# Kernel tuning notes

Hardware: AMD Instinct MI355X
Metric: run time of the kernel (lower is better)

## Reference

```python
import jax, jax.numpy as jnp
import numpy as np

RADIUS = 2.0  # ball-query radius (float forward arg in the original; fixed here)


def _conv1x1(x, W, b):
    # 1x1 Conv2D over NHWC == per-point linear layer
    return jnp.einsum('bmsc,cd->bmsd', x, W) + b


def _ball_query(xyz, new_xyz, radius, nsample):
    """For each cluster center, take the first (by index) nsample points within
    radius, padding with the first found neighbor (TF ball-query semantics).
    xyz: (B,N,3), new_xyz: (B,M,3) -> idx (B,M,nsample) int32."""
    N = xyz.shape[1]
    d2 = jnp.sum((new_xyz[:, :, None, :] - xyz[:, None, :, :]) ** 2, axis=-1)  # (B,M,N)
    valid = d2 < radius * radius
    key = jnp.where(valid, jnp.arange(N, dtype=jnp.int32)[None, None, :], N)
    order = jnp.argsort(key, axis=-1)[..., :nsample]          # (B,M,nsample)
    skey = jnp.take_along_axis(key, order, axis=-1)
    idx = jnp.where(skey < N, order, order[..., :1])          # pad with first neighbor
    return idx


def setup_inputs() -> dict:
    key = jax.random.key(0)
    ks = jax.random.split(key, 8)
    B, N = 8, 8192
    xyz = jax.random.normal(ks[0], (B, N, 3), dtype=jnp.float32)

    def w(k, cin, cout):
        return (jax.random.normal(k, (cin, cout), dtype=jnp.float32) / np.sqrt(cin)).astype(jnp.float32)

    z = lambda c: jnp.zeros((c,), jnp.float32)
    inp = {
        'xyz': xyz,
        'W1': w(ks[1], 3, 64),    'b1': z(64),
        'W2': w(ks[2], 64, 128),  'b2': z(128),
        'W3': w(ks[3], 128, 256), 'b3': z(256),
        'W4': w(ks[4], 256, 128), 'b4': z(128),
        'W5': w(ks[5], 128, 64),  'b5': z(64),
        'Wa': w(ks[6], 64, 1),    'ba': z(1),
        'Wo': w(ks[7], 64, 2),    'bo': z(2),
        'num_clusters': 512,
        'num_samples': 64,
    }
    return inp


def reference(xyz, W1, b1, W2, b2, W3, b3, W4, b4, W5, b5, Wa, ba, Wo, bo,
              num_clusters, num_samples):
    # sample cluster centers (deterministic stand-in for random subsampling)
    new_xyz = xyz[:, :num_clusters]                                    # (B,M,3)
    idx = _ball_query(xyz, new_xyz, RADIUS, num_samples)               # (B,M,S)
    grouped = jax.vmap(lambda pts, i: pts[i])(xyz, idx)                # (B,M,S,3)
    g = (grouped - new_xyz[:, :, None, :]) / RADIUS                    # normalize_radius

    # shared per-point MLP (1x1 convs, relu)
    h = jax.nn.relu(_conv1x1(g, W1, b1))
    h = jax.nn.relu(_conv1x1(h, W2, b2))
    h = jax.nn.relu(_conv1x1(h, W3, b3))
    # MaxPoolAxis: max over samples, keepdims
    h = jnp.max(h, axis=2, keepdims=True)                              # (B,M,1,256)
    # mlp2 convs (linear, no activation in source)
    h = _conv1x1(h, W4, b4)
    h = _conv1x1(h, W5, b5)                                            # (B,M,1,64)

    attention = jax.nn.softplus(_conv1x1(h, Wa, ba))[:, :, 0, 0]       # (B,M)
    o = _conv1x1(h, Wo, bo)[:, :, 0, :]                                # (B,M,2)
    o = o / jnp.sqrt(jnp.maximum(jnp.sum(o * o, axis=-1, keepdims=True), 1e-8))
    orientation = jnp.arctan2(o[..., 1], o[..., 0])                    # (B,M)
    return new_xyz, idx, attention, orientation
```

## Files before the change

kernel.cpp:

```cpp
#include <hip/hip_runtime.h>
#include <math.h>

#define BB 8
#define NN 8192
#define MM 512
#define SS 64
#define NCLUST (BB*MM)

#define OUT_IDX   (BB*MM*3)
#define OUT_ATT   (OUT_IDX + BB*MM*SS)
#define OUT_ORI   (OUT_ATT + BB*MM)

#define WS_W3 8192

typedef short v8s __attribute__((ext_vector_type(8)));
typedef float v4f __attribute__((ext_vector_type(4)));

static __device__ __forceinline__ unsigned short f2bf(float x) {
    unsigned int u = __float_as_uint(x);
    u += 0x7FFFu + ((u >> 16) & 1u);
    return (unsigned short)(u >> 16);
}

__global__ void pack_weights(const float* __restrict__ W2,
                             const float* __restrict__ W3,
                             unsigned short* __restrict__ ws)
{
    const int gid = blockIdx.x * 256 + threadIdx.x;
    const float* W; unsigned short* dst; int N, kt, nt, lane;
    if (gid < 1024) {
        W = W2; N = 128;
        const int tile = gid >> 6; lane = gid & 63;
        kt = tile >> 3; nt = tile & 7;
        dst = ws + (size_t)(tile * 64 + lane) * 8;
    } else {
        const int g = gid - 1024;
        W = W3; N = 256;
        const int tile = g >> 6; lane = g & 63;
        kt = tile >> 4; nt = tile & 15;
        dst = ws + WS_W3 + (size_t)(tile * 64 + lane) * 8;
    }
    const int k0 = kt * 32 + (lane >> 4) * 8;
    const int n  = nt * 16 + (lane & 15);
    union { unsigned short u[8]; v8s v; } f;
    #pragma unroll
    for (int j = 0; j < 8; ++j) f.u[j] = f2bf(W[(k0 + j) * N + n]);
    *(v8s*)dst = f.v;
}

__global__ __launch_bounds__(256, 4) void feat3d_fused(
    const float* __restrict__ xyz,
    const float* __restrict__ W1, const float* __restrict__ b1,
    const float* __restrict__ b2, const float* __restrict__ b3,
    const unsigned short* __restrict__ Wp,
    const float* __restrict__ W4, const float* __restrict__ b4,
    const float* __restrict__ W5, const float* __restrict__ b5,
    const float* __restrict__ Wa, const float* __restrict__ ba,
    const float* __restrict__ Wo, const float* __restrict__ bo,
    float* __restrict__ out)
{
    __shared__ __align__(16) unsigned char lds[24576];
    unsigned short* a2p = (unsigned short*)lds;
    unsigned short* a3p = (unsigned short*)(lds + 8192);
    float* smallf       = (float*)(lds + 8192);
    int* ls_idx         = (int*)(lds + 10240);
    unsigned long long* ls_mask = (unsigned long long*)(lds + 10496);

    float* ls_g  = smallf;
    float* ls_w1 = smallf + 256;

    float* vbuf   = (float*)lds;
    float* h4part = (float*)(lds + 1024);
    float* h4f    = (float*)(lds + 5120);
    float* h5p    = (float*)(lds + 5632);

    const int t   = threadIdx.x;
    const int wv  = t >> 6;
    const int l   = t & 63;
    const int q   = l >> 4;
    const int r16 = l & 15;
    const int blk = blockIdx.x;
    const int b   = blk >> 9;
    const int m   = blk & 511;
    const float* xb = xyz + (size_t)b * (NN * 3);

    const v8s* W2f = (const v8s*)Wp;
    v8s bfr[2][2];
    #pragma unroll
    for (int kt = 0; kt < 2; ++kt)
        #pragma unroll
        for (int ni = 0; ni < 2; ++ni)
            bfr[kt][ni] = W2f[(kt*8 + 2*wv + ni)*64 + l];

    const float cx = xb[m*3+0], cy = xb[m*3+1], cz = xb[m*3+2];

    if (t < 3) out[(b*MM + m)*3 + t] = xb[m*3 + t];

    if (t < 64) {
        ls_w1[t*4+0] = W1[t];
        ls_w1[t*4+1] = W1[64 + t];
        ls_w1[t*4+2] = W1[128 + t];
        ls_w1[t*4+3] = b1[t];
    }

    int cnt = 0;
    {
        int base = 0, pb = 0;
        while (base < NN && cnt < SS) {
            const int j = base + t;
            const float dx = xb[j*3+0] - cx;
            const float dy = xb[j*3+1] - cy;
            const float dz = xb[j*3+2] - cz;
            const float d2 = __fadd_rn(__fadd_rn(__fmul_rn(dx,dx), __fmul_rn(dy,dy)),
                                       __fmul_rn(dz,dz));
            const bool valid = d2 < 4.0f;
            const unsigned long long mask = __ballot(valid);
            if (l == 0) ls_mask[pb*4 + wv] = mask;
            __syncthreads();
            const unsigned long long m0 = ls_mask[pb*4+0], m1 = ls_mask[pb*4+1],
                                     m2 = ls_mask[pb*4+2], m3 = ls_mask[pb*4+3];
            int below = __popcll(mask & ((1ull << l) - 1ull));
            if (wv > 0) below += (int)__popcll(m0);
            if (wv > 1) below += (int)__popcll(m1);
            if (wv > 2) below += (int)__popcll(m2);
            const int pos = cnt + below;
            if (valid && pos < SS) {
                ls_idx[pos]   = j;
                ls_g[pos*4+0] = dx * 0.5f;
                ls_g[pos*4+1] = dy * 0.5f;
                ls_g[pos*4+2] = dz * 0.5f;
            }
            cnt += (int)(__popcll(m0) + __popcll(m1) + __popcll(m2) + __popcll(m3));
            if (cnt > SS) cnt = SS;
            base += 256;
            pb ^= 1;
        }
    }
    __syncthreads();
    if (t < SS && t >= cnt) {
        ls_idx[t]   = ls_idx[0];
        ls_g[t*4+0] = ls_g[0];
        ls_g[t*4+1] = ls_g[1];
        ls_g[t*4+2] = ls_g[2];
    }
    __syncthreads();
    if (t < 64) out[OUT_IDX + (b*MM + m)*SS + t] = (float)ls_idx[t];

    {
        const int s = wv*16 + r16;
        const float4 g4 = *(const float4*)&ls_g[s*4];
        #pragma unroll
        for (int kt = 0; kt < 2; ++kt) {
            union { unsigned short u[8]; v8s v; } fr;
            #pragma unroll
            for (int j = 0; j < 8; ++j) {
                const int c = kt*32 + q*8 + j;
                const float4 w = *(const float4*)&ls_w1[c*4];
                const float h = fmaf(g4.x, w.x, fmaf(g4.y, w.y, fmaf(g4.z, w.z, w.w)));
                fr.u[j] = f2bf(fmaxf(h, 0.f));
            }
            *(v8s*)&a2p[((kt*4 + wv)*64 + l)*8] = fr.v;
        }
    }
    __syncthreads();

    {
        const v4f z = {0.f, 0.f, 0.f, 0.f};
        v4f acc[4][2];
        #pragma unroll
        for (int mt = 0; mt < 4; ++mt) { acc[mt][0] = z; acc[mt][1] = z; }

        #pragma unroll
        for (int kt = 0; kt < 2; ++kt)
            #pragma unroll
            for (int mt = 0; mt < 4; ++mt) {
                const v8s a = *(const v8s*)&a2p[((kt*4 + mt)*64 + l)*8];
                #pragma unroll
                for (int ni = 0; ni < 2; ++ni)
                    acc[mt][ni] = __builtin_amdgcn_mfma_f32_16x16x32_bf16(
                        a, bfr[kt][ni], acc[mt][ni], 0, 0, 0);
            }

        #pragma unroll
        for (int ni = 0; ni < 2; ++ni) {
            const int c2  = (2*wv + ni)*16 + r16;
            const float bias = b2[c2];
            const int kt3 = c2 >> 5;
            const int lhi = ((c2 >> 3) & 3) << 4;
            const int j3  = c2 & 7;
            #pragma unroll
            for (int mt = 0; mt < 4; ++mt)
                #pragma unroll
                for (int rg = 0; rg < 4; ++rg) {
                    const float h = fmaxf(acc[mt][ni][rg] + bias, 0.f);
                    const int s15 = q*4 + rg;
                    a3p[((kt3*4 + mt)*64 + (lhi | s15))*8 + j3] = f2bf(h);
                }
        }
    }
    __syncthreads();

    {
        const v8s* W3f = (const v8s*)(Wp + WS_W3);

        #pragma unroll
        for (int np = 0; np < 2; ++np) {
            const int nt0 = 4*wv + 2*np;
            const v4f z = {0.f, 0.f, 0.f, 0.f};
            v4f acc[4][2];
            #pragma unroll
            for (int mt = 0; mt < 4; ++mt) { acc[mt][0] = z; acc[mt][1] = z; }

            v8s bb0 = W3f[(0*16 + nt0    )*64 + l];
            v8s bb1 = W3f[(0*16 + nt0 + 1)*64 + l];
            #pragma unroll
            for (int kt = 0; kt < 4; ++kt) {
                v8s a[4];
                #pragma unroll
                for (int mt = 0; mt < 4; ++mt)
                    a[mt] = *(const v8s*)&a3p[((kt*4 + mt)*64 + l)*8];
                v8s nb0, nb1;
                if (kt < 3) {
                    nb0 = W3f[((kt+1)*16 + nt0    )*64 + l];
                    nb1 = W3f[((kt+1)*16 + nt0 + 1)*64 + l];
                }
                #pragma unroll
                for (int mt = 0; mt < 4; ++mt) {
                    acc[mt][0] = __builtin_amdgcn_mfma_f32_16x16x32_bf16(
                        a[mt], bb0, acc[mt][0], 0, 0, 0);
                    acc[mt][1] = __builtin_amdgcn_mfma_f32_16x16x32_bf16(
                        a[mt], bb1, acc[mt][1], 0, 0, 0);
                }
                if (kt < 3) { bb0 = nb0; bb1 = nb1; }
            }

            #pragma unroll
            for (int ni = 0; ni < 2; ++ni) {
                float mx = acc[0][ni][0];
                #pragma unroll
                for (int mt = 0; mt < 4; ++mt)
                    #pragma unroll
                    for (int rg = 0; rg < 4; ++rg)
                        mx = fmaxf(mx, acc[mt][ni][rg]);
                mx = fmaxf(mx, __shfl_xor(mx, 16));
                mx = fmaxf(mx, __shfl_xor(mx, 32));
                if (q == 0) {
                    const int c = (nt0 + ni)*16 + r16;
                    vbuf[c] = fmaxf(mx + b3[c], 0.f);
                }
            }
        }
    }
    __syncthreads();

    {
        const int cgp = t & 31;
        const int kp  = t >> 5;
        const float4* W4v = (const float4*)W4;
        float4 acc = make_float4(0.f, 0.f, 0.f, 0.f);
        const int kbase = kp * 32;
        #pragma unroll 4
        for (int kk = 0; kk < 32; ++kk) {
            const int k = kbase + kk;
            const float4 w = W4v[k*32 + cgp];
            const float vv = vbuf[k];
            acc.x = fmaf(vv, w.x, acc.x);
            acc.y = fmaf(vv, w.y, acc.y);
            acc.z = fmaf(vv, w.z, acc.z);
            acc.w = fmaf(vv, w.w, acc.w);
        }
        *(float4*)&h4part[kp*128 + cgp*4] = acc;
    }
    __syncthreads();
    if (t < 128) {
        float s = b4[t];
        #pragma unroll
        for (int kp = 0; kp < 8; ++kp) s += h4part[kp*128 + t];
        h4f[t] = s;
    }
    __syncthreads();

    {
        const int c5 = t & 63;
        const int kq = t >> 6;
        const float* W5c = W5 + c5;
        float acc = 0.f;
        for (int k = kq*32; k < kq*32 + 32; k += 4) {
            const float4 hh = *(const float4*)&h4f[k];
            acc = fmaf(hh.x, W5c[(k+0)*64],
                  fmaf(hh.y, W5c[(k+1)*64],
                  fmaf(hh.z, W5c[(k+2)*64],
                  fmaf(hh.w, W5c[(k+3)*64], acc))));
        }
        h5p[t] = acc;
    }
    __syncthreads();

    if (t < 64) {
        const float h5v = h5p[t] + h5p[64 + t] + h5p[128 + t] + h5p[192 + t] + b5[t];
        float va = h5v * Wa[t];
        float v0 = h5v * Wo[2*t + 0];
        float v1 = h5v * Wo[2*t + 1];
        #pragma unroll
        for (int off = 32; off > 0; off >>= 1) {
            va += __shfl_down(va, off);
            v0 += __shfl_down(v0, off);
            v1 += __shfl_down(v1, off);
        }
        if (t == 0) {
            const float a = va + ba[0];
            out[OUT_ATT + blk] = fmaxf(a, 0.f) + log1pf(expf(-fabsf(a)));
            out[OUT_ORI + blk] = atan2f(v1 + bo[1], v0 + bo[0]);
        }
    }
}

extern "C" void kernel_launch(void* const* d_in, const int* in_sizes, int n_in,
                              void* d_out, int out_size, void* d_ws, size_t ws_size,
                              hipStream_t stream) {
    const float* xyz = (const float*)d_in[0];
    const float* W1  = (const float*)d_in[1];
    const float* b1  = (const float*)d_in[2];
    const float* W2  = (const float*)d_in[3];
    const float* b2  = (const float*)d_in[4];
    const float* W3  = (const float*)d_in[5];
    const float* b3  = (const float*)d_in[6];
    const float* W4  = (const float*)d_in[7];
    const float* b4  = (const float*)d_in[8];
    const float* W5  = (const float*)d_in[9];
    const float* b5  = (const float*)d_in[10];
    const float* Wa  = (const float*)d_in[11];
    const float* ba  = (const float*)d_in[12];
    const float* Wo  = (const float*)d_in[13];
    const float* bo  = (const float*)d_in[14];

    unsigned short* ws = (unsigned short*)d_ws;

    pack_weights<<<dim3(20), dim3(256), 0, stream>>>(W2, W3, ws);
    feat3d_fused<<<dim3(NCLUST), dim3(256), 0, stream>>>(
        xyz, W1, b1, b2, b3, ws, W4, b4, W5, b5, Wa, ba, Wo, bo, (float*)d_out);
}
```

Before: 133.7 us.

## Split fused kernel; batch MLP tail over four clusters per block

Splits the fused kernel into a front kernel (ball query, MLP layers 1-3, max-pool) and a tail kernel. The front writes each cluster's pooled 256-vector as bf16 to workspace. The tail processes four clusters per block so every W4/W5 weight load is reused across four clusters, cutting redundant weight traffic and shrinking the front kernel's serial tail. The cost is an extra launch, a global round trip, and bf16 rounding of the pooled features before the linear layers.

Result: faster. 130.9 us (-2.1%).

```diff
diff --git a/kernel.cpp b/kernel.cpp
--- a/kernel.cpp
+++ b/kernel.cpp
@@ -6,12 +6,14 @@
 #define MM 512
 #define SS 64
 #define NCLUST (BB*MM)
+#define TCL 4
 
 #define OUT_IDX   (BB*MM*3)
 #define OUT_ATT   (OUT_IDX + BB*MM*SS)
 #define OUT_ORI   (OUT_ATT + BB*MM)
 
 #define WS_W3 8192
+#define WS_V  40960
 
 typedef short v8s __attribute__((ext_vector_type(8)));
 typedef float v4f __attribute__((ext_vector_type(4)));
@@ -48,15 +50,12 @@
     *(v8s*)dst = f.v;
 }
 
-__global__ __launch_bounds__(256, 4) void feat3d_fused(
+__global__ __launch_bounds__(256, 4) void feat3d_front(
     const float* __restrict__ xyz,
     const float* __restrict__ W1, const float* __restrict__ b1,
     const float* __restrict__ b2, const float* __restrict__ b3,
     const unsigned short* __restrict__ Wp,
-    const float* __restrict__ W4, const float* __restrict__ b4,
-    const float* __restrict__ W5, const float* __restrict__ b5,
-    const float* __restrict__ Wa, const float* __restrict__ ba,
-    const float* __restrict__ Wo, const float* __restrict__ bo,
+    unsigned short* __restrict__ vdst,
     float* __restrict__ out)
 {
     __shared__ __align__(16) unsigned char lds[24576];
@@ -68,11 +67,6 @@
 
     float* ls_g  = smallf;
     float* ls_w1 = smallf + 256;
-
-    float* vbuf   = (float*)lds;
-    float* h4part = (float*)(lds + 1024);
-    float* h4f    = (float*)(lds + 5120);
-    float* h5p    = (float*)(lds + 5632);
 
     const int t   = threadIdx.x;
     const int wv  = t >> 6;
@@ -202,6 +196,7 @@
 
     {
         const v8s* W3f = (const v8s*)(Wp + WS_W3);
+        unsigned short* vrow = vdst + (size_t)blk * 256;
 
         #pragma unroll
         for (int np = 0; np < 2; ++np) {
@@ -246,9 +241,36 @@
                 mx = fmaxf(mx, __shfl_xor(mx, 32));
                 if (q == 0) {
                     const int c = (nt0 + ni)*16 + r16;
-                    vbuf[c] = fmaxf(mx + b3[c], 0.f);
+                    vrow[c] = f2bf(fmaxf(mx + b3[c], 0.f));
                 }
             }
+        }
+    }
+}
+
+__global__ __launch_bounds__(256) void feat3d_tail(
+    const unsigned short* __restrict__ vsrc,
+    const float* __restrict__ W4, const float* __restrict__ b4,
+    const float* __restrict__ W5, const float* __restrict__ b5,
+    const float* __restrict__ Wa, const float* __restrict__ ba,
+    const float* __restrict__ Wo, const float* __restrict__ bo,
+    float* __restrict__ out)
+{
+    __shared__ __align__(16) float V[TCL*256];
+    __shared__ __align__(16) float h4part[8][TCL*128];
+    __shared__ __align__(16) float h4f[TCL*128];
+    __shared__ __align__(16) float h5p[4][TCL*64];
+
+    const int t   = threadIdx.x;
+    const int cl0 = blockIdx.x * TCL;
+
+    {
+        const uint4 r = ((const uint4*)(vsrc + (size_t)cl0 * 256))[t];
+        const unsigned int u[4] = {r.x, r.y, r.z, r.w};
+        #pragma unroll
+        for (int j = 0; j < 4; ++j) {
+            V[t*8 + 2*j]     = __uint_as_float(u[j] << 16);
+            V[t*8 + 2*j + 1] = __uint_as_float(u[j] & 0xFFFF0000u);
         }
     }
     __syncthreads();
@@ -257,60 +279,84 @@
         const int cgp = t & 31;
         const int kp  = t >> 5;
         const float4* W4v = (const float4*)W4;
-        float4 acc = make_float4(0.f, 0.f, 0.f, 0.f);
+        float4 a0 = make_float4(0.f,0.f,0.f,0.f);
+        float4 a1 = make_float4(0.f,0.f,0.f,0.f);
+        float4 a2 = make_float4(0.f,0.f,0.f,0.f);
+        float4 a3 = make_float4(0.f,0.f,0.f,0.f);
         const int kbase = kp * 32;
         #pragma unroll 4
         for (int kk = 0; kk < 32; ++kk) {
             const int k = kbase + kk;
             const float4 w = W4v[k*32 + cgp];
-            const float vv = vbuf[k];
-            acc.x = fmaf(vv, w.x, acc.x);
-            acc.y = fmaf(vv, w.y, acc.y);
-            acc.z = fmaf(vv, w.z, acc.z);
-            acc.w = fmaf(vv, w.w, acc.w);
-        }
-        *(float4*)&h4part[kp*128 + cgp*4] = acc;
-    }
-    __syncthreads();
-    if (t < 128) {
-        float s = b4[t];
-        #pragma unroll
-        for (int kp = 0; kp < 8; ++kp) s += h4part[kp*128 + t];
-        h4f[t] = s;
+            const float v0 = V[0*256 + k];
+            const float v1 = V[1*256 + k];
+            const float v2 = V[2*256 + k];
+            const float v3 = V[3*256 + k];
+            a0.x = fmaf(v0, w.x, a0.x); a0.y = fmaf(v0, w.y, a0.y);
+            a0.z = fmaf(v0, w.z, a0.z); a0.w = fmaf(v0, w.w, a0.w);
+            a1.x = fmaf(v1, w.x, a1.x); a1.y = fmaf(v1, w.y, a1.y);
+            a1.z = fmaf(v1, w.z, a1.z); a1.w = fmaf(v1, w.w, a1.w);
+            a2.x = fmaf(v2, w.x, a2.x); a2.y = fmaf(v2, w.y, a2.y);
+            a2.z = fmaf(v2, w.z, a2.z); a2.w = fmaf(v2, w.w, a2.w);
+            a3.x = fmaf(v3, w.x, a3.x); a3.y = fmaf(v3, w.y, a3.y);
+            a3.z = fmaf(v3, w.z, a3.z); a3.w = fmaf(v3, w.w, a3.w);
+        }
+        *(float4*)&h4part[kp][0*128 + cgp*4] = a0;
+        *(float4*)&h4part[kp][1*128 + cgp*4] = a1;
+        *(float4*)&h4part[kp][2*128 + cgp*4] = a2;
+        *(float4*)&h4part[kp][3*128 + cgp*4] = a3;
+    }
+    __syncthreads();
+
+    #pragma unroll
+    for (int idx = t; idx < TCL*128; idx += 256) {
+        const int c = idx & 127;
+        float s = b4[c];
+        #pragma unroll
+        for (int kp = 0; kp < 8; ++kp) s += h4part[kp][idx];
+        h4f[idx] = s;
     }
     __syncthreads();
 
     {
         const int c5 = t & 63;
         const int kq = t >> 6;
-        const float* W5c = W5 + c5;
-        float acc = 0.f;
-        for (int k = kq*32; k < kq*32 + 32; k += 4) {
-            const float4 hh = *(const float4*)&h4f[k];
-            acc = fmaf(hh.x, W5c[(k+0)*64],
-                  fmaf(hh.y, W5c[(k+1)*64],
-                  fmaf(hh.z, W5c[(k+2)*64],
-                  fmaf(hh.w, W5c[(k+3)*64], acc))));
-        }
-        h5p[t] = acc;
-    }
-    __syncthreads();
-
-    if (t < 64) {
-        const float h5v = h5p[t] + h5p[64 + t] + h5p[128 + t] + h5p[192 + t] + b5[t];
-        float va = h5v * Wa[t];
-        float v0 = h5v * Wo[2*t + 0];
-        float v1 = h5v * Wo[2*t + 1];
+        float s0 = 0.f, s1 = 0.f, s2 = 0.f, s3 = 0.f;
+        #pragma unroll 4
+        for (int kk = 0; kk < 32; ++kk) {
+            const int k = kq*32 + kk;
+            const float w = W5[k*64 + c5];
+            s0 = fmaf(h4f[0*128 + k], w, s0);
+            s1 = fmaf(h4f[1*128 + k], w, s1);
+            s2 = fmaf(h4f[2*128 + k], w, s2);
+            s3 = fmaf(h4f[3*128 + k], w, s3);
+        }
+        h5p[kq][0*64 + c5] = s0;
+        h5p[kq][1*64 + c5] = s1;
+        h5p[kq][2*64 + c5] = s2;
+        h5p[kq][3*64 + c5] = s3;
+    }
+    __syncthreads();
+
+    {
+        const int wv = t >> 6, l = t & 63;
+        float h5v = b5[l];
+        #pragma unroll
+        for (int kq = 0; kq < 4; ++kq) h5v += h5p[kq][wv*64 + l];
+        float va = h5v * Wa[l];
+        float v0 = h5v * Wo[2*l + 0];
+        float v1 = h5v * Wo[2*l + 1];
         #pragma unroll
         for (int off = 32; off > 0; off >>= 1) {
             va += __shfl_down(va, off);
             v0 += __shfl_down(v0, off);
             v1 += __shfl_down(v1, off);
         }
-        if (t == 0) {
+        if (l == 0) {
+            const int cg = cl0 + wv;
             const float a = va + ba[0];
-            out[OUT_ATT + blk] = fmaxf(a, 0.f) + log1pf(expf(-fabsf(a)));
-            out[OUT_ORI + blk] = atan2f(v1 + bo[1], v0 + bo[0]);
+            out[OUT_ATT + cg] = fmaxf(a, 0.f) + log1pf(expf(-fabsf(a)));
+            out[OUT_ORI + cg] = atan2f(v1 + bo[1], v0 + bo[0]);
         }
     }
 }
@@ -337,6 +383,8 @@
     unsigned short* ws = (unsigned short*)d_ws;
 
     pack_weights<<<dim3(20), dim3(256), 0, stream>>>(W2, W3, ws);
-    feat3d_fused<<<dim3(NCLUST), dim3(256), 0, stream>>>(
-        xyz, W1, b1, b2, b3, ws, W4, b4, W5, b5, Wa, ba, Wo, bo, (float*)d_out);
-}
+    feat3d_front<<<dim3(NCLUST), dim3(256), 0, stream>>>(
+        xyz, W1, b1, b2, b3, ws, ws + WS_V, (float*)d_out);
+    feat3d_tail<<<dim3(NCLUST/TCL), dim3(256), 0, stream>>>(
+        ws + WS_V, W4, b4, W5, b5, Wa, ba, Wo, bo, (float*)d_out);
+}
```
